# Kernel tuning notes

Measured on AMD Instinct MI355X. Metric: run time of the kernel, lower is better.

Reference implementation:

```python
import jax, jax.numpy as jnp
import numpy as np

B, T, N, C = 1, 2, 10000, 64
H, Co = 4, 64
E = 160000
NEG_SLOPE = 0.2
LN_EPS = 1e-5


def setup_inputs() -> dict:
    key = jax.random.key(0)
    ks = jax.random.split(key, 8)
    s_in = 1.0 / np.sqrt(C)
    s_att = 1.0 / np.sqrt(Co)
    s_proj = 1.0 / np.sqrt(H * Co)
    return {
        "x": jax.random.normal(ks[0], (B, T, N, C), jnp.float32),
        "edge_index": jax.random.randint(ks[1], (2, E), 0, N, dtype=jnp.int32),
        "W_l": jax.random.normal(ks[2], (C, H * Co), jnp.float32) * s_in,
        "b_l": jnp.zeros((H * Co,), jnp.float32),
        "W_r": jax.random.normal(ks[3], (C, H * Co), jnp.float32) * s_in,
        "b_r": jnp.zeros((H * Co,), jnp.float32),
        "att": jax.random.normal(ks[4], (H, Co), jnp.float32) * s_att,
        "bias": jnp.zeros((H * Co,), jnp.float32),
        "W_proj": jax.random.normal(ks[5], (H * Co, Co), jnp.float32) * s_proj,
        "b_proj": jnp.zeros((Co,), jnp.float32),
        "ln_gamma": jnp.ones((Co,), jnp.float32),
        "ln_beta": jnp.zeros((Co,), jnp.float32),
    }


def reference(x, edge_index, W_l, b_l, W_r, b_r, att, bias, W_proj, b_proj, ln_gamma, ln_beta):
    src, dst = edge_index[0], edge_index[1]
    # node transforms: [B,T,N,H,Co]
    x_l = (x @ W_l + b_l).reshape(B, T, N, H, Co)
    x_r = (x @ W_r + b_r).reshape(B, T, N, H, Co)
    # per-edge gathers: [B,T,E,H,Co]
    x_j = x_l[:, :, src]  # source-side features (messages)
    x_i = x_r[:, :, dst]  # target-side features
    m = jax.nn.leaky_relu(x_i + x_j, NEG_SLOPE)
    alpha = jnp.einsum('bteho,ho->bteh', m, att)  # [B,T,E,H]
    # segment softmax over edges grouped by target node (edge axis leading)
    a = jnp.moveaxis(alpha, 2, 0)  # [E,B,T,H]
    amax = jax.lax.stop_gradient(jax.ops.segment_max(a, dst, num_segments=N))
    a = jnp.exp(a - amax[dst])
    denom = jax.ops.segment_sum(a, dst, num_segments=N)
    attn = a / denom[dst]  # [E,B,T,H]
    # weighted messages scattered to target nodes
    msg = jnp.moveaxis(x_j, 2, 0) * attn[..., None]  # [E,B,T,H,Co]
    agg = jax.ops.segment_sum(msg, dst, num_segments=N)  # [N,B,T,H,Co]
    out = jnp.moveaxis(agg, 0, 2).reshape(B, T, N, H * Co) + bias
    x_mha = jax.nn.relu(out)
    # projection + identity residual (in_channels == out_channels)
    x_sam = x_mha @ W_proj + b_proj + x
    mu = jnp.mean(x_sam, axis=-1, keepdims=True)
    var = jnp.var(x_sam, axis=-1, keepdims=True)
    y = (x_sam - mu) * jax.lax.rsqrt(var + LN_EPS) * ln_gamma + ln_beta
    return jax.nn.relu(y)
```

## Files before the change

kernel.cpp:

```cpp
#include <hip/hip_runtime.h>

#define T_  2
#define N_  10000
#define C_  64
#define H_  4
#define Co_ 64
#define E_  160000
#define HC_ 256
#define NEG_SLOPE 0.2f
#define LN_EPS 1e-5f

__device__ __forceinline__ float lrelu(float v) {
    return fmaxf(v, NEG_SLOPE * v);
}
__device__ __forceinline__ float bf2f(unsigned short u) {
    return __uint_as_float((unsigned)u << 16);
}
__device__ __forceinline__ unsigned short f2bf(float f) {
    const unsigned u = __float_as_uint(f);
    return (unsigned short)((u + 0x7FFFu + ((u >> 16) & 1u)) >> 16);
}

__global__ __launch_bounds__(256) void gemm_lr(
        const float* __restrict__ x, const float* __restrict__ Wl,
        const float* __restrict__ bl, const float* __restrict__ Wr,
        const float* __restrict__ br, unsigned short* __restrict__ xlb,
        float* __restrict__ xr) {
    __shared__ float4 xs[16 * 16];
    const int tid  = threadIdx.x;
    const int r0   = blockIdx.x * 16;
    const int half = tid >> 7;
    const int q    = tid & 127;
    const int mat  = q >> 6;
    const int col4 = q & 63;
    const float* W  = mat ? Wr : Wl;
    const float* bv = mat ? br : bl;

    xs[tid] = ((const float4*)(x + (size_t)r0 * C_))[tid];
    __syncthreads();

    const float4 b4 = ((const float4*)bv)[col4];
    float4 acc[8];
    #pragma unroll
    for (int r = 0; r < 8; ++r) acc[r] = b4;

    const int rbase = half * 8;
    #pragma unroll 2
    for (int c4 = 0; c4 < 16; ++c4) {
        const float4 w0 = ((const float4*)(W + (size_t)(c4 * 4 + 0) * HC_))[col4];
        const float4 w1 = ((const float4*)(W + (size_t)(c4 * 4 + 1) * HC_))[col4];
        const float4 w2 = ((const float4*)(W + (size_t)(c4 * 4 + 2) * HC_))[col4];
        const float4 w3 = ((const float4*)(W + (size_t)(c4 * 4 + 3) * HC_))[col4];
        #pragma unroll
        for (int r = 0; r < 8; ++r) {
            const float4 xv = xs[(rbase + r) * 16 + c4];
            acc[r].x = fmaf(xv.x, w0.x, acc[r].x);
            acc[r].y = fmaf(xv.x, w0.y, acc[r].y);
            acc[r].z = fmaf(xv.x, w0.z, acc[r].z);
            acc[r].w = fmaf(xv.x, w0.w, acc[r].w);
            acc[r].x = fmaf(xv.y, w1.x, acc[r].x);
            acc[r].y = fmaf(xv.y, w1.y, acc[r].y);
            acc[r].z = fmaf(xv.y, w1.z, acc[r].z);
            acc[r].w = fmaf(xv.y, w1.w, acc[r].w);
            acc[r].x = fmaf(xv.z, w2.x, acc[r].x);
            acc[r].y = fmaf(xv.z, w2.y, acc[r].y);
            acc[r].z = fmaf(xv.z, w2.z, acc[r].z);
            acc[r].w = fmaf(xv.z, w2.w, acc[r].w);
            acc[r].x = fmaf(xv.w, w3.x, acc[r].x);
            acc[r].y = fmaf(xv.w, w3.y, acc[r].y);
            acc[r].z = fmaf(xv.w, w3.z, acc[r].z);
            acc[r].w = fmaf(xv.w, w3.w, acc[r].w);
        }
    }
    if (mat) {
        #pragma unroll
        for (int r = 0; r < 8; ++r)
            ((float4*)(xr + (size_t)(r0 + rbase + r) * HC_))[col4] = acc[r];
    } else {
        #pragma unroll
        for (int r = 0; r < 8; ++r) {
            ushort4 u;
            u.x = f2bf(acc[r].x); u.y = f2bf(acc[r].y);
            u.z = f2bf(acc[r].z); u.w = f2bf(acc[r].w);
            ((ushort4*)(xlb + (size_t)(r0 + rbase + r) * HC_))[col4] = u;
        }
    }
}

__global__ __launch_bounds__(256) void hist_kernel(
        const int* __restrict__ dst, int* __restrict__ count) {
    const int e = blockIdx.x * 256 + threadIdx.x;
    if (e < E_) atomicAdd(&count[dst[e]], 1);
}

__global__ __launch_bounds__(1024) void scan_kernel(
        const int* __restrict__ count, int* __restrict__ row_start) {
    __shared__ int wsum[16];
    const int tid  = threadIdx.x;
    const int lane = tid & 63, wave = tid >> 6;
    const int base = tid * 10;
    int local[10];
    int s = 0;
    #pragma unroll
    for (int i = 0; i < 10; ++i) {
        const int idx = base + i;
        const int v = (idx < N_) ? count[idx] : 0;
        local[i] = s;
        s += v;
    }
    int incl = s;
    #pragma unroll
    for (int off = 1; off < 64; off <<= 1) {
        const int u = __shfl_up(incl, off, 64);
        if (lane >= off) incl += u;
    }
    if (lane == 63) wsum[wave] = incl;
    __syncthreads();
    if (wave == 0 && lane < 16) {
        const int v = wsum[lane];
        int iv = v;
        #pragma unroll
        for (int off = 1; off < 16; off <<= 1) {
            const int u = __shfl_up(iv, off, 64);
            if (lane >= off) iv += u;
        }
        wsum[lane] = iv - v;
        if (lane == 15) row_start[N_] = iv;
    }
    __syncthreads();
    const int tpre = wsum[wave] + (incl - s);
    #pragma unroll
    for (int i = 0; i < 10; ++i) {
        const int idx = base + i;
        if (idx < N_) row_start[idx] = tpre + local[i];
    }
}

__global__ __launch_bounds__(256) void scatter_kernel(
        const int* __restrict__ src, const int* __restrict__ dst,
        const int* __restrict__ row_start, int* __restrict__ cursor,
        int* __restrict__ perm_src) {
    const int e = blockIdx.x * 256 + threadIdx.x;
    if (e >= E_) return;
    const int d = dst[e];
    const int pos = row_start[d] + atomicAdd(&cursor[d], 1);
    perm_src[pos] = src[e];
}

__global__ __launch_bounds__(256) void node_agg(
        const unsigned short* __restrict__ xlb, const float* __restrict__ xr,
        const float* __restrict__ att, const int* __restrict__ perm_src,
        const int* __restrict__ row_start, float* __restrict__ agg) {
    const int wid  = blockIdx.x * 4 + (threadIdx.x >> 6);
    const int lane = threadIdx.x & 63;
    const int t = wid / N_, n = wid % N_;
    const int beg = row_start[n], end = row_start[n + 1];
    const float4 xi = ((const float4*)&xr[(size_t)wid * HC_])[lane];
    const float4 av = ((const float4*)att)[lane];
    const unsigned short* xlt = xlb + (size_t)t * N_ * HC_;

    float m = -INFINITY, s = 0.f;
    float4 acc = make_float4(0.f, 0.f, 0.f, 0.f);

    for (int base = beg; base < end; base += 64) {
        const int cnt = min(64, end - base);
        const int myidx = (lane < cnt) ? perm_src[base + lane] : 0;
        for (int k = 0; k < cnt; k += 4) {
            const int i0 = __shfl(myidx, k + 0, 64);
            const int i1 = __shfl(myidx, k + 1, 64);
            const int i2 = __shfl(myidx, k + 2, 64);
            const int i3 = __shfl(myidx, k + 3, 64);
            const ushort4 u0 = ((const ushort4*)&xlt[(size_t)i0 * HC_])[lane];
            const ushort4 u1 = ((const ushort4*)&xlt[(size_t)i1 * HC_])[lane];
            const ushort4 u2 = ((const ushort4*)&xlt[(size_t)i2 * HC_])[lane];
            const ushort4 u3 = ((const ushort4*)&xlt[(size_t)i3 * HC_])[lane];
            const float4 c0 = make_float4(bf2f(u0.x), bf2f(u0.y), bf2f(u0.z), bf2f(u0.w));
            const float4 c1 = make_float4(bf2f(u1.x), bf2f(u1.y), bf2f(u1.z), bf2f(u1.w));
            const float4 c2 = make_float4(bf2f(u2.x), bf2f(u2.y), bf2f(u2.z), bf2f(u2.w));
            const float4 c3 = make_float4(bf2f(u3.x), bf2f(u3.y), bf2f(u3.z), bf2f(u3.w));
            float p0 =      lrelu(xi.x + c0.x) * av.x;
            p0 = fmaf(lrelu(xi.y + c0.y), av.y, p0);
            p0 = fmaf(lrelu(xi.z + c0.z), av.z, p0);
            p0 = fmaf(lrelu(xi.w + c0.w), av.w, p0);
            float p1 =      lrelu(xi.x + c1.x) * av.x;
            p1 = fmaf(lrelu(xi.y + c1.y), av.y, p1);
            p1 = fmaf(lrelu(xi.z + c1.z), av.z, p1);
            p1 = fmaf(lrelu(xi.w + c1.w), av.w, p1);
            float p2 =      lrelu(xi.x + c2.x) * av.x;
            p2 = fmaf(lrelu(xi.y + c2.y), av.y, p2);
            p2 = fmaf(lrelu(xi.z + c2.z), av.z, p2);
            p2 = fmaf(lrelu(xi.w + c2.w), av.w, p2);
            float p3 =      lrelu(xi.x + c3.x) * av.x;
            p3 = fmaf(lrelu(xi.y + c3.y), av.y, p3);
            p3 = fmaf(lrelu(xi.z + c3.z), av.z, p3);
            p3 = fmaf(lrelu(xi.w + c3.w), av.w, p3);
            #pragma unroll
            for (int o = 1; o < 16; o <<= 1) {
                p0 += __shfl_xor(p0, o, 64);
                p1 += __shfl_xor(p1, o, 64);
                p2 += __shfl_xor(p2, o, 64);
                p3 += __shfl_xor(p3, o, 64);
            }
            if (k + 1 >= cnt) p1 = -INFINITY;
            if (k + 2 >= cnt) p2 = -INFINITY;
            if (k + 3 >= cnt) p3 = -INFINITY;
            const float gm = fmaxf(fmaxf(p0, p1), fmaxf(p2, p3));
            const float m_new = fmaxf(m, gm);
            const float sc = __expf(m - m_new);
            const float w0 = __expf(p0 - m_new);
            const float w1 = __expf(p1 - m_new);
            const float w2 = __expf(p2 - m_new);
            const float w3 = __expf(p3 - m_new);
            s = fmaf(s, sc, w0 + w1 + w2 + w3);
            acc.x = fmaf(acc.x, sc,
                    fmaf(w0, c0.x, fmaf(w1, c1.x, fmaf(w2, c2.x, w3 * c3.x))));
            acc.y = fmaf(acc.y, sc,
                    fmaf(w0, c0.y, fmaf(w1, c1.y, fmaf(w2, c2.y, w3 * c3.y))));
            acc.z = fmaf(acc.z, sc,
                    fmaf(w0, c0.z, fmaf(w1, c1.z, fmaf(w2, c2.z, w3 * c3.z))));
            acc.w = fmaf(acc.w, sc,
                    fmaf(w0, c0.w, fmaf(w1, c1.w, fmaf(w2, c2.w, w3 * c3.w))));
            m = m_new;
        }
    }
    if (end > beg) {
        const float inv = 1.f / s;
        acc.x *= inv; acc.y *= inv; acc.z *= inv; acc.w *= inv;
    }
    ((float4*)&agg[(size_t)wid * HC_])[lane] = acc;
}

__global__ __launch_bounds__(256) void epilogue(
        const float* __restrict__ agg, const float* __restrict__ bias,
        const float* __restrict__ Wp, const float* __restrict__ bp,
        const float* __restrict__ x, const float* __restrict__ gamma,
        const float* __restrict__ beta, float* __restrict__ out) {
    __shared__ float sh[32 * HC_];
    const int r0  = blockIdx.x * 32;
    const int tid = threadIdx.x;
    #pragma unroll
    for (int i = 0; i < 8; ++i) {
        const int slot = i * 256 + tid;
        const int r = slot >> 6, f4 = slot & 63;
        float4 v = ((const float4*)&agg[(size_t)(r0 + r) * HC_])[f4];
        const float4 b = ((const float4*)bias)[f4];
        v.x = fmaxf(v.x + b.x, 0.f); v.y = fmaxf(v.y + b.y, 0.f);
        v.z = fmaxf(v.z + b.z, 0.f); v.w = fmaxf(v.w + b.w, 0.f);
        ((float4*)sh)[slot] = v;
    }
    __syncthreads();
    const int wave = tid >> 6, o = tid & 63;
    const int rbase = wave * 8;
    const float bpo = bp[o];
    float acc[8];
    #pragma unroll
    for (int r = 0; r < 8; ++r)
        acc[r] = bpo + x[(size_t)(r0 + rbase + r) * C_ + o];
    for (int k = 0; k < HC_; k += 4) {
        const float w0 = Wp[(k + 0) * Co_ + o];
        const float w1 = Wp[(k + 1) * Co_ + o];
        const float w2 = Wp[(k + 2) * Co_ + o];
        const float w3 = Wp[(k + 3) * Co_ + o];
        #pragma unroll
        for (int r = 0; r < 8; ++r) {
            const float4 s4 = ((const float4*)&sh[(rbase + r) * HC_])[k >> 2];
            acc[r] = fmaf(s4.x, w0, acc[r]);
            acc[r] = fmaf(s4.y, w1, acc[r]);
            acc[r] = fmaf(s4.z, w2, acc[r]);
            acc[r] = fmaf(s4.w, w3, acc[r]);
        }
    }
    const float go = gamma[o], bo = beta[o];
    #pragma unroll
    for (int r = 0; r < 8; ++r) {
        float s1 = acc[r];
        #pragma unroll
        for (int off = 1; off < 64; off <<= 1) s1 += __shfl_xor(s1, off, 64);
        const float mu = s1 * (1.f / 64.f);
        const float dv = acc[r] - mu;
        float s2 = dv * dv;
        #pragma unroll
        for (int off = 1; off < 64; off <<= 1) s2 += __shfl_xor(s2, off, 64);
        const float var = s2 * (1.f / 64.f);
        const float y = dv * rsqrtf(var + LN_EPS) * go + bo;
        out[(size_t)(r0 + rbase + r) * C_ + o] = fmaxf(y, 0.f);
    }
}

extern "C" void kernel_launch(void* const* d_in, const int* in_sizes, int n_in,
                              void* d_out, int out_size, void* d_ws, size_t ws_size,
                              hipStream_t stream) {
    const float* x    = (const float*)d_in[0];
    const int*   ei   = (const int*)  d_in[1];
    const float* Wl   = (const float*)d_in[2];
    const float* bl   = (const float*)d_in[3];
    const float* Wr   = (const float*)d_in[4];
    const float* br   = (const float*)d_in[5];
    const float* att  = (const float*)d_in[6];
    const float* bias = (const float*)d_in[7];
    const float* Wp   = (const float*)d_in[8];
    const float* bp   = (const float*)d_in[9];
    const float* gam  = (const float*)d_in[10];
    const float* bet  = (const float*)d_in[11];
    const int* src = ei;
    const int* dst = ei + E_;

    float* ws = (float*)d_ws;
    unsigned short* xlb = (unsigned short*)ws;
    float* xr  = (float*)(xlb + (size_t)T_ * N_ * HC_);
    float* agg = xr + (size_t)T_ * N_ * HC_;
    int* row_start = (int*)(agg + (size_t)T_ * N_ * HC_);
    int* count     = row_start + (N_ + 1);
    int* cursor    = count + N_;
    int* perm_src  = cursor + N_;

    hipMemsetAsync(count, 0, 2 * N_ * sizeof(int), stream);

    hist_kernel   <<<(E_ + 255) / 256, 256, 0, stream>>>(dst, count);
    scan_kernel   <<<1, 1024, 0, stream>>>(count, row_start);
    scatter_kernel<<<(E_ + 255) / 256, 256, 0, stream>>>(src, dst, row_start,
                                                         cursor, perm_src);
    gemm_lr <<<T_ * N_ / 16, 256, 0, stream>>>(x, Wl, bl, Wr, br, xlb, xr);
    node_agg<<<T_ * N_ / 4,  256, 0, stream>>>(xlb, xr, att, perm_src,
                                               row_start, agg);
    epilogue<<<T_ * N_ / 32, 256, 0, stream>>>(agg, bias, Wp, bp, x, gam, bet,
                                               (float*)d_out);
}
```

Measured before the change: 190.1 us.

## Fuse edge histogram and scan into GEMM launch via extra block

The memset, global-atomic histogram, single-block scan and node GEMM are merged into one kernel. The GEMM blocks keep their old code, and one extra block builds the destination-count histogram in shared memory with LDS atomics, scans it, and writes both row_start and the cursor base. The scatter kernel then only does one atomic on the pre-offset cursor. This removes three launches and a memset, but one block now does all 160k edge atomics serially and may stretch the critical path. The 40 KB static shared allocation also applies to every GEMM block, which can reduce GEMM occupancy.

```diff
diff --git a/kernel.cpp b/kernel.cpp
--- a/kernel.cpp
+++ b/kernel.cpp
@@ -9,6 +9,7 @@
 #define HC_ 256
 #define NEG_SLOPE 0.2f
 #define LN_EPS 1e-5f
+#define GEMM_BLOCKS (T_ * N_ / 16)
 
 __device__ __forceinline__ float lrelu(float v) {
     return fmaxf(v, NEG_SLOPE * v);
@@ -21,129 +22,135 @@
     return (unsigned short)((u + 0x7FFFu + ((u >> 16) & 1u)) >> 16);
 }
 
-__global__ __launch_bounds__(256) void gemm_lr(
+__global__ __launch_bounds__(256) void fused_pre(
         const float* __restrict__ x, const float* __restrict__ Wl,
         const float* __restrict__ bl, const float* __restrict__ Wr,
         const float* __restrict__ br, unsigned short* __restrict__ xlb,
-        float* __restrict__ xr) {
-    __shared__ float4 xs[16 * 16];
-    const int tid  = threadIdx.x;
-    const int r0   = blockIdx.x * 16;
-    const int half = tid >> 7;
-    const int q    = tid & 127;
-    const int mat  = q >> 6;
-    const int col4 = q & 63;
-    const float* W  = mat ? Wr : Wl;
-    const float* bv = mat ? br : bl;
-
-    xs[tid] = ((const float4*)(x + (size_t)r0 * C_))[tid];
-    __syncthreads();
-
-    const float4 b4 = ((const float4*)bv)[col4];
-    float4 acc[8];
-    #pragma unroll
-    for (int r = 0; r < 8; ++r) acc[r] = b4;
-
-    const int rbase = half * 8;
-    #pragma unroll 2
-    for (int c4 = 0; c4 < 16; ++c4) {
-        const float4 w0 = ((const float4*)(W + (size_t)(c4 * 4 + 0) * HC_))[col4];
-        const float4 w1 = ((const float4*)(W + (size_t)(c4 * 4 + 1) * HC_))[col4];
-        const float4 w2 = ((const float4*)(W + (size_t)(c4 * 4 + 2) * HC_))[col4];
-        const float4 w3 = ((const float4*)(W + (size_t)(c4 * 4 + 3) * HC_))[col4];
-        #pragma unroll
-        for (int r = 0; r < 8; ++r) {
-            const float4 xv = xs[(rbase + r) * 16 + c4];
-            acc[r].x = fmaf(xv.x, w0.x, acc[r].x);
-            acc[r].y = fmaf(xv.x, w0.y, acc[r].y);
-            acc[r].z = fmaf(xv.x, w0.z, acc[r].z);
-            acc[r].w = fmaf(xv.x, w0.w, acc[r].w);
-            acc[r].x = fmaf(xv.y, w1.x, acc[r].x);
-            acc[r].y = fmaf(xv.y, w1.y, acc[r].y);
-            acc[r].z = fmaf(xv.y, w1.z, acc[r].z);
-            acc[r].w = fmaf(xv.y, w1.w, acc[r].w);
-            acc[r].x = fmaf(xv.z, w2.x, acc[r].x);
-            acc[r].y = fmaf(xv.z, w2.y, acc[r].y);
-            acc[r].z = fmaf(xv.z, w2.z, acc[r].z);
-            acc[r].w = fmaf(xv.z, w2.w, acc[r].w);
-            acc[r].x = fmaf(xv.w, w3.x, acc[r].x);
-            acc[r].y = fmaf(xv.w, w3.y, acc[r].y);
-            acc[r].z = fmaf(xv.w, w3.z, acc[r].z);
-            acc[r].w = fmaf(xv.w, w3.w, acc[r].w);
-        }
-    }
-    if (mat) {
-        #pragma unroll
-        for (int r = 0; r < 8; ++r)
-            ((float4*)(xr + (size_t)(r0 + rbase + r) * HC_))[col4] = acc[r];
+        float* __restrict__ xr, const int* __restrict__ dst,
+        int* __restrict__ row_start, int* __restrict__ cursor) {
+    __shared__ __align__(16) char smem[40992];
+    const int tid = threadIdx.x;
+
+    if (blockIdx.x < GEMM_BLOCKS) {
+        float4* xs = (float4*)smem;
+        const int r0   = blockIdx.x * 16;
+        const int half = tid >> 7;
+        const int q    = tid & 127;
+        const int mat  = q >> 6;
+        const int col4 = q & 63;
+        const float* W  = mat ? Wr : Wl;
+        const float* bv = mat ? br : bl;
+
+        xs[tid] = ((const float4*)(x + (size_t)r0 * C_))[tid];
+        __syncthreads();
+
+        const float4 b4 = ((const float4*)bv)[col4];
+        float4 acc[8];
+        #pragma unroll
+        for (int r = 0; r < 8; ++r) acc[r] = b4;
+
+        const int rbase = half * 8;
+        #pragma unroll 2
+        for (int c4 = 0; c4 < 16; ++c4) {
+            const float4 w0 = ((const float4*)(W + (size_t)(c4 * 4 + 0) * HC_))[col4];
+            const float4 w1 = ((const float4*)(W + (size_t)(c4 * 4 + 1) * HC_))[col4];
+            const float4 w2 = ((const float4*)(W + (size_t)(c4 * 4 + 2) * HC_))[col4];
+            const float4 w3 = ((const float4*)(W + (size_t)(c4 * 4 + 3) * HC_))[col4];
+            #pragma unroll
+            for (int r = 0; r < 8; ++r) {
+                const float4 xv = xs[(rbase + r) * 16 + c4];
+                acc[r].x = fmaf(xv.x, w0.x, acc[r].x);
+                acc[r].y = fmaf(xv.x, w0.y, acc[r].y);
+                acc[r].z = fmaf(xv.x, w0.z, acc[r].z);
+                acc[r].w = fmaf(xv.x, w0.w, acc[r].w);
+                acc[r].x = fmaf(xv.y, w1.x, acc[r].x);
+                acc[r].y = fmaf(xv.y, w1.y, acc[r].y);
+                acc[r].z = fmaf(xv.y, w1.z, acc[r].z);
+                acc[r].w = fmaf(xv.y, w1.w, acc[r].w);
+                acc[r].x = fmaf(xv.z, w2.x, acc[r].x);
+                acc[r].y = fmaf(xv.z, w2.y, acc[r].y);
+                acc[r].z = fmaf(xv.z, w2.z, acc[r].z);
+                acc[r].w = fmaf(xv.z, w2.w, acc[r].w);
+                acc[r].x = fmaf(xv.w, w3.x, acc[r].x);
+                acc[r].y = fmaf(xv.w, w3.y, acc[r].y);
+                acc[r].z = fmaf(xv.w, w3.z, acc[r].z);
+                acc[r].w = fmaf(xv.w, w3.w, acc[r].w);
+            }
+        }
+        if (mat) {
+            #pragma unroll
+            for (int r = 0; r < 8; ++r)
+                ((float4*)(xr + (size_t)(r0 + rbase + r) * HC_))[col4] = acc[r];
+        } else {
+            #pragma unroll
+            for (int r = 0; r < 8; ++r) {
+                ushort4 u;
+                u.x = f2bf(acc[r].x); u.y = f2bf(acc[r].y);
+                u.z = f2bf(acc[r].z); u.w = f2bf(acc[r].w);
+                ((ushort4*)(xlb + (size_t)(r0 + rbase + r) * HC_))[col4] = u;
+            }
+        }
     } else {
-        #pragma unroll
-        for (int r = 0; r < 8; ++r) {
-            ushort4 u;
-            u.x = f2bf(acc[r].x); u.y = f2bf(acc[r].y);
-            u.z = f2bf(acc[r].z); u.w = f2bf(acc[r].w);
-            ((ushort4*)(xlb + (size_t)(r0 + rbase + r) * HC_))[col4] = u;
-        }
-    }
-}
-
-__global__ __launch_bounds__(256) void hist_kernel(
-        const int* __restrict__ dst, int* __restrict__ count) {
-    const int e = blockIdx.x * 256 + threadIdx.x;
-    if (e < E_) atomicAdd(&count[dst[e]], 1);
-}
-
-__global__ __launch_bounds__(1024) void scan_kernel(
-        const int* __restrict__ count, int* __restrict__ row_start) {
-    __shared__ int wsum[16];
-    const int tid  = threadIdx.x;
-    const int lane = tid & 63, wave = tid >> 6;
-    const int base = tid * 10;
-    int local[10];
-    int s = 0;
-    #pragma unroll
-    for (int i = 0; i < 10; ++i) {
-        const int idx = base + i;
-        const int v = (idx < N_) ? count[idx] : 0;
-        local[i] = s;
-        s += v;
-    }
-    int incl = s;
-    #pragma unroll
-    for (int off = 1; off < 64; off <<= 1) {
-        const int u = __shfl_up(incl, off, 64);
-        if (lane >= off) incl += u;
-    }
-    if (lane == 63) wsum[wave] = incl;
-    __syncthreads();
-    if (wave == 0 && lane < 16) {
-        const int v = wsum[lane];
-        int iv = v;
-        #pragma unroll
-        for (int off = 1; off < 16; off <<= 1) {
-            const int u = __shfl_up(iv, off, 64);
-            if (lane >= off) iv += u;
-        }
-        wsum[lane] = iv - v;
-        if (lane == 15) row_start[N_] = iv;
-    }
-    __syncthreads();
-    const int tpre = wsum[wave] + (incl - s);
-    #pragma unroll
-    for (int i = 0; i < 10; ++i) {
-        const int idx = base + i;
-        if (idx < N_) row_start[idx] = tpre + local[i];
+        int* cnt  = (int*)smem;
+        int* wsum = (int*)(smem + 40000);
+        const int lane = tid & 63, wave = tid >> 6;
+
+        for (int i = tid; i < N_; i += 256) cnt[i] = 0;
+        __syncthreads();
+        const int4* d4 = (const int4*)dst;
+        for (int i = tid; i < E_ / 4; i += 256) {
+            const int4 v = d4[i];
+            atomicAdd(&cnt[v.x], 1);
+            atomicAdd(&cnt[v.y], 1);
+            atomicAdd(&cnt[v.z], 1);
+            atomicAdd(&cnt[v.w], 1);
+        }
+        __syncthreads();
+        const int base = tid * 40;
+        int s = 0;
+        for (int i = 0; i < 40; ++i) {
+            const int idx = base + i;
+            if (idx < N_) s += cnt[idx];
+        }
+        int incl = s;
+        #pragma unroll
+        for (int off = 1; off < 64; off <<= 1) {
+            const int u = __shfl_up(incl, off, 64);
+            if (lane >= off) incl += u;
+        }
+        if (lane == 63) wsum[wave] = incl;
+        __syncthreads();
+        if (wave == 0 && lane < 4) {
+            const int v = wsum[lane];
+            int iv = v;
+            #pragma unroll
+            for (int off = 1; off < 4; off <<= 1) {
+                const int u = __shfl_up(iv, off, 64);
+                if (lane >= off) iv += u;
+            }
+            wsum[lane] = iv - v;
+            if (lane == 3) row_start[N_] = iv;
+        }
+        __syncthreads();
+        int run = wsum[wave] + (incl - s);
+        for (int i = 0; i < 40; ++i) {
+            const int idx = base + i;
+            if (idx < N_) {
+                const int c = cnt[idx];
+                row_start[idx] = run;
+                cursor[idx]    = run;
+                run += c;
+            }
+        }
     }
 }
 
 __global__ __launch_bounds__(256) void scatter_kernel(
         const int* __restrict__ src, const int* __restrict__ dst,
-        const int* __restrict__ row_start, int* __restrict__ cursor,
-        int* __restrict__ perm_src) {
+        int* __restrict__ cursor, int* __restrict__ perm_src) {
     const int e = blockIdx.x * 256 + threadIdx.x;
     if (e >= E_) return;
-    const int d = dst[e];
-    const int pos = row_start[d] + atomicAdd(&cursor[d], 1);
+    const int pos = atomicAdd(&cursor[dst[e]], 1);
     perm_src[pos] = src[e];
 }
 
@@ -310,17 +317,13 @@
     float* xr  = (float*)(xlb + (size_t)T_ * N_ * HC_);
     float* agg = xr + (size_t)T_ * N_ * HC_;
     int* row_start = (int*)(agg + (size_t)T_ * N_ * HC_);
-    int* count     = row_start + (N_ + 1);
-    int* cursor    = count + N_;
+    int* cursor    = row_start + (N_ + 1);
     int* perm_src  = cursor + N_;
 
-    hipMemsetAsync(count, 0, 2 * N_ * sizeof(int), stream);
-
-    hist_kernel   <<<(E_ + 255) / 256, 256, 0, stream>>>(dst, count);
-    scan_kernel   <<<1, 1024, 0, stream>>>(count, row_start);
-    scatter_kernel<<<(E_ + 255) / 256, 256, 0, stream>>>(src, dst, row_start,
-                                                         cursor, perm_src);
-    gemm_lr <<<T_ * N_ / 16, 256, 0, stream>>>(x, Wl, bl, Wr, br, xlb, xr);
+    fused_pre<<<GEMM_BLOCKS + 1, 256, 0, stream>>>(
+        x, Wl, bl, Wr, br, xlb, xr, dst, row_start, cursor);
+    scatter_kernel<<<(E_ + 255) / 256, 256, 0, stream>>>(src, dst, cursor,
+                                                         perm_src);
     node_agg<<<T_ * N_ / 4,  256, 0, stream>>>(xlb, xr, att, perm_src,
                                                row_start, agg);
     epilogue<<<T_ * N_ / 32, 256, 0, stream>>>(agg, bias, Wp, bp, x, gam, bet,
```

Result: slower. 215.9 us (+13.5%).

## Fuse edge scatter into GEMM launch, seed cursor in scan, store agg as bf16

Applied to the files above, without the earlier changes.

The scan kernel now writes the row starts directly into the cursor array, so the scatter no longer reads row_start and only half the memset is needed. The scatter blocks are merged into the node-transform GEMM launch, which removes one launch and lets the two independent jobs overlap on the device. The aggregated features are stored as bf16 instead of fp32, halving the traffic between node_agg and the epilogue at the cost of some precision.

```diff
diff --git a/kernel.cpp b/kernel.cpp
--- a/kernel.cpp
+++ b/kernel.cpp
@@ -9,6 +9,8 @@
 #define HC_ 256
 #define NEG_SLOPE 0.2f
 #define LN_EPS 1e-5f
+#define SCAT_BLOCKS ((E_ + 255) / 256)
+#define GEMM_BLOCKS (T_ * N_ / 16)
 
 __device__ __forceinline__ float lrelu(float v) {
     return fmaxf(v, NEG_SLOPE * v);
@@ -21,14 +23,78 @@
     return (unsigned short)((u + 0x7FFFu + ((u >> 16) & 1u)) >> 16);
 }
 
-__global__ __launch_bounds__(256) void gemm_lr(
+__global__ __launch_bounds__(256) void hist_kernel(
+        const int* __restrict__ dst, int* __restrict__ count) {
+    const int e = blockIdx.x * 256 + threadIdx.x;
+    if (e < E_) atomicAdd(&count[dst[e]], 1);
+}
+
+__global__ __launch_bounds__(1024) void scan_kernel(
+        const int* __restrict__ count, int* __restrict__ row_start,
+        int* __restrict__ cursor) {
+    __shared__ int wsum[16];
+    const int tid  = threadIdx.x;
+    const int lane = tid & 63, wave = tid >> 6;
+    const int base = tid * 10;
+    int local[10];
+    int s = 0;
+    #pragma unroll
+    for (int i = 0; i < 10; ++i) {
+        const int idx = base + i;
+        const int v = (idx < N_) ? count[idx] : 0;
+        local[i] = s;
+        s += v;
+    }
+    int incl = s;
+    #pragma unroll
+    for (int off = 1; off < 64; off <<= 1) {
+        const int u = __shfl_up(incl, off, 64);
+        if (lane >= off) incl += u;
+    }
+    if (lane == 63) wsum[wave] = incl;
+    __syncthreads();
+    if (wave == 0 && lane < 16) {
+        const int v = wsum[lane];
+        int iv = v;
+        #pragma unroll
+        for (int off = 1; off < 16; off <<= 1) {
+            const int u = __shfl_up(iv, off, 64);
+            if (lane >= off) iv += u;
+        }
+        wsum[lane] = iv - v;
+        if (lane == 15) row_start[N_] = iv;
+    }
+    __syncthreads();
+    const int tpre = wsum[wave] + (incl - s);
+    #pragma unroll
+    for (int i = 0; i < 10; ++i) {
+        const int idx = base + i;
+        if (idx < N_) {
+            const int st = tpre + local[i];
+            row_start[idx] = st;
+            cursor[idx]    = st;
+        }
+    }
+}
+
+__global__ __launch_bounds__(256) void scat_gemm(
+        const int* __restrict__ src, const int* __restrict__ dst,
+        int* __restrict__ cursor, int* __restrict__ perm_src,
         const float* __restrict__ x, const float* __restrict__ Wl,
         const float* __restrict__ bl, const float* __restrict__ Wr,
         const float* __restrict__ br, unsigned short* __restrict__ xlb,
         float* __restrict__ xr) {
+    const int tid = threadIdx.x;
+    if (blockIdx.x < SCAT_BLOCKS) {
+        const int e = blockIdx.x * 256 + tid;
+        if (e < E_) {
+            const int pos = atomicAdd(&cursor[dst[e]], 1);
+            perm_src[pos] = src[e];
+        }
+        return;
+    }
     __shared__ float4 xs[16 * 16];
-    const int tid  = threadIdx.x;
-    const int r0   = blockIdx.x * 16;
+    const int r0   = (blockIdx.x - SCAT_BLOCKS) * 16;
     const int half = tid >> 7;
     const int q    = tid & 127;
     const int mat  = q >> 6;
@@ -87,70 +153,10 @@
     }
 }
 
-__global__ __launch_bounds__(256) void hist_kernel(
-        const int* __restrict__ dst, int* __restrict__ count) {
-    const int e = blockIdx.x * 256 + threadIdx.x;
-    if (e < E_) atomicAdd(&count[dst[e]], 1);
-}
-
-__global__ __launch_bounds__(1024) void scan_kernel(
-        const int* __restrict__ count, int* __restrict__ row_start) {
-    __shared__ int wsum[16];
-    const int tid  = threadIdx.x;
-    const int lane = tid & 63, wave = tid >> 6;
-    const int base = tid * 10;
-    int local[10];
-    int s = 0;
-    #pragma unroll
-    for (int i = 0; i < 10; ++i) {
-        const int idx = base + i;
-        const int v = (idx < N_) ? count[idx] : 0;
-        local[i] = s;
-        s += v;
-    }
-    int incl = s;
-    #pragma unroll
-    for (int off = 1; off < 64; off <<= 1) {
-        const int u = __shfl_up(incl, off, 64);
-        if (lane >= off) incl += u;
-    }
-    if (lane == 63) wsum[wave] = incl;
-    __syncthreads();
-    if (wave == 0 && lane < 16) {
-        const int v = wsum[lane];
-        int iv = v;
-        #pragma unroll
-        for (int off = 1; off < 16; off <<= 1) {
-            const int u = __shfl_up(iv, off, 64);
-            if (lane >= off) iv += u;
-        }
-        wsum[lane] = iv - v;
-        if (lane == 15) row_start[N_] = iv;
-    }
-    __syncthreads();
-    const int tpre = wsum[wave] + (incl - s);
-    #pragma unroll
-    for (int i = 0; i < 10; ++i) {
-        const int idx = base + i;
-        if (idx < N_) row_start[idx] = tpre + local[i];
-    }
-}
-
-__global__ __launch_bounds__(256) void scatter_kernel(
-        const int* __restrict__ src, const int* __restrict__ dst,
-        const int* __restrict__ row_start, int* __restrict__ cursor,
-        int* __restrict__ perm_src) {
-    const int e = blockIdx.x * 256 + threadIdx.x;
-    if (e >= E_) return;
-    const int d = dst[e];
-    const int pos = row_start[d] + atomicAdd(&cursor[d], 1);
-    perm_src[pos] = src[e];
-}
-
 __global__ __launch_bounds__(256) void node_agg(
         const unsigned short* __restrict__ xlb, const float* __restrict__ xr,
         const float* __restrict__ att, const int* __restrict__ perm_src,
-        const int* __restrict__ row_start, float* __restrict__ agg) {
+        const int* __restrict__ row_start, unsigned short* __restrict__ aggb) {
     const int wid  = blockIdx.x * 4 + (threadIdx.x >> 6);
     const int lane = threadIdx.x & 63;
     const int t = wid / N_, n = wid % N_;
@@ -227,11 +233,14 @@
         const float inv = 1.f / s;
         acc.x *= inv; acc.y *= inv; acc.z *= inv; acc.w *= inv;
     }
-    ((float4*)&agg[(size_t)wid * HC_])[lane] = acc;
+    ushort4 o4;
+    o4.x = f2bf(acc.x); o4.y = f2bf(acc.y);
+    o4.z = f2bf(acc.z); o4.w = f2bf(acc.w);
+    ((ushort4*)&aggb[(size_t)wid * HC_])[lane] = o4;
 }
 
 __global__ __launch_bounds__(256) void epilogue(
-        const float* __restrict__ agg, const float* __restrict__ bias,
+        const unsigned short* __restrict__ aggb, const float* __restrict__ bias,
         const float* __restrict__ Wp, const float* __restrict__ bp,
         const float* __restrict__ x, const float* __restrict__ gamma,
         const float* __restrict__ beta, float* __restrict__ out) {
@@ -242,10 +251,11 @@
     for (int i = 0; i < 8; ++i) {
         const int slot = i * 256 + tid;
         const int r = slot >> 6, f4 = slot & 63;
-        float4 v = ((const float4*)&agg[(size_t)(r0 + r) * HC_])[f4];
+        const ushort4 u = ((const ushort4*)&aggb[(size_t)(r0 + r) * HC_])[f4];
         const float4 b = ((const float4*)bias)[f4];
-        v.x = fmaxf(v.x + b.x, 0.f); v.y = fmaxf(v.y + b.y, 0.f);
-        v.z = fmaxf(v.z + b.z, 0.f); v.w = fmaxf(v.w + b.w, 0.f);
+        float4 v;
+        v.x = fmaxf(bf2f(u.x) + b.x, 0.f); v.y = fmaxf(bf2f(u.y) + b.y, 0.f);
+        v.z = fmaxf(bf2f(u.z) + b.z, 0.f); v.w = fmaxf(bf2f(u.w) + b.w, 0.f);
         ((float4*)sh)[slot] = v;
     }
     __syncthreads();
@@ -305,24 +315,23 @@
     const int* src = ei;
     const int* dst = ei + E_;
 
-    float* ws = (float*)d_ws;
-    unsigned short* xlb = (unsigned short*)ws;
-    float* xr  = (float*)(xlb + (size_t)T_ * N_ * HC_);
-    float* agg = xr + (size_t)T_ * N_ * HC_;
-    int* row_start = (int*)(agg + (size_t)T_ * N_ * HC_);
+    char* ws = (char*)d_ws;
+    unsigned short* xlb  = (unsigned short*)ws;
+    float*          xr   = (float*)(xlb + (size_t)T_ * N_ * HC_);
+    unsigned short* aggb = (unsigned short*)(xr + (size_t)T_ * N_ * HC_);
+    int* row_start = (int*)(aggb + (size_t)T_ * N_ * HC_);
     int* count     = row_start + (N_ + 1);
     int* cursor    = count + N_;
     int* perm_src  = cursor + N_;
 
-    hipMemsetAsync(count, 0, 2 * N_ * sizeof(int), stream);
-
-    hist_kernel   <<<(E_ + 255) / 256, 256, 0, stream>>>(dst, count);
-    scan_kernel   <<<1, 1024, 0, stream>>>(count, row_start);
-    scatter_kernel<<<(E_ + 255) / 256, 256, 0, stream>>>(src, dst, row_start,
-                                                         cursor, perm_src);
-    gemm_lr <<<T_ * N_ / 16, 256, 0, stream>>>(x, Wl, bl, Wr, br, xlb, xr);
-    node_agg<<<T_ * N_ / 4,  256, 0, stream>>>(xlb, xr, att, perm_src,
-                                               row_start, agg);
-    epilogue<<<T_ * N_ / 32, 256, 0, stream>>>(agg, bias, Wp, bp, x, gam, bet,
-                                               (float*)d_out);
-}
+    hipMemsetAsync(count, 0, N_ * sizeof(int), stream);
+
+    hist_kernel<<<SCAT_BLOCKS, 256, 0, stream>>>(dst, count);
+    scan_kernel<<<1, 1024, 0, stream>>>(count, row_start, cursor);
+    scat_gemm  <<<SCAT_BLOCKS + GEMM_BLOCKS, 256, 0, stream>>>(
+        src, dst, cursor, perm_src, x, Wl, bl, Wr, br, xlb, xr);
+    node_agg   <<<T_ * N_ / 4,  256, 0, stream>>>(xlb, xr, att, perm_src,
+                                                  row_start, aggb);
+    epilogue   <<<T_ * N_ / 32, 256, 0, stream>>>(aggb, bias, Wp, bp, x,
+                                                  gam, bet, (float*)d_out);
+}
```

Result: no change. 187.6 us, median of 2 (-1.3%).
